# Performance work log

Measured on AMD Instinct MI355X. Metric: run time of the kernel, lower is better.

Reference implementation:

```python
import jax, jax.numpy as jnp
import numpy as np

B = 32768      # batch
D = 2          # input_dim
H = 2048       # hidden_dim
NQ = 4         # qubits


def setup_inputs() -> dict:
    key = jax.random.key(0)
    ks = jax.random.split(key, 14)

    def lin(k, fan_in, fan_out):
        # kaiming-uniform-ish init like nn.Linear
        bound = 1.0 / np.sqrt(fan_in)
        kw, kb = jax.random.split(k)
        W = jax.random.uniform(kw, (fan_in, fan_out), jnp.float32, -bound, bound)
        b = jax.random.uniform(kb, (fan_out,), jnp.float32, -bound, bound)
        return W, b

    x = jax.random.normal(ks[0], (B, D), jnp.float32)
    W1, b1 = lin(ks[1], D + NQ, H)      # core Linear 1
    W2, b2 = lin(ks[2], H, H)           # core Linear 2
    Wc, bc = lin(ks[3], H, 1)           # classifier
    Wr1, br1 = lin(ks[4], D, 8)
    Wr2, br2 = lin(ks[5], 8, 4)
    Wr3, br3 = lin(ks[6], 4, 1)
    return dict(x=x, W1=W1, b1=b1, W2=W2, b2=b2, Wc=Wc, bc=bc,
                Wr1=Wr1, br1=br1, Wr2=Wr2, br2=br2, Wr3=Wr3, br3=br3)


def _quantum_feature_map(x):
    # Exact closed form of: RY(x_i) on 4 qubits from |0000>, CNOT(0,1), CNOT(2,3),
    # expval(PauliZ(i)). Padding with zeros -> cos(0)=1 on unused wires.
    xq = jnp.pad(x, ((0, 0), (0, NQ - x.shape[1])))  # [B,4]
    c = jnp.cos(xq)
    return jnp.stack([c[:, 0], c[:, 0] * c[:, 1], c[:, 2], c[:, 2] * c[:, 3]], axis=1)


def reference(x, W1, b1, W2, b2, Wc, bc, Wr1, br1, Wr2, br2, Wr3, br3):
    qfeat = _quantum_feature_map(x)               # [B,4]
    concat = jnp.concatenate([x, qfeat], axis=1)  # [B, D+4]
    h = jnp.tanh(concat @ W1 + b1)                # [B,H]
    h = jnp.tanh(h @ W2 + b2)                     # [B,H]
    logits = h @ Wc + bc                          # [B,1]
    r = jnp.tanh(x @ Wr1 + br1)
    r = jnp.tanh(r @ Wr2 + br2)
    risk = r @ Wr3 + br3                          # [B,1]
    return logits, risk
```

## Files before the change

### kernel.cpp

```cpp
#include <hip/hip_runtime.h>
#include <hip/hip_bf16.h>
#include <stdint.h>

#define B_ROWS 32768
#define HID    2048
#define K_DIM  2048

#define BM 256
#define BN 256
#define BKB 128
#define NKT (K_DIM / BKB)
#define NS  4
#define NU  (NS * NKT)
#define ASTEP ((size_t)8192 * K_DIM)

#define SCALE_W   5747.3639f
#define DEQUANT   1.3700225e-6f

#define L1_BLOCKS (B_ROWS / 32)
#define TR_BLOCKS ((HID/32)*(K_DIM/32))

typedef int  int4v __attribute__((ext_vector_type(4)));
typedef char char8 __attribute__((ext_vector_type(8)));

__device__ __forceinline__ float fast_tanh(float x) {
    float e = __expf(2.0f * x);
    return 1.0f - 2.0f * __builtin_amdgcn_rcpf(e + 1.0f);
}

__device__ __forceinline__ void gl_lds16(const void* g, void* l) {
    __builtin_amdgcn_global_load_lds(
        (const __attribute__((address_space(1))) void*)(uintptr_t)g,
        (__attribute__((address_space(3))) void*)(uint32_t)(uintptr_t)l,
        16, 0, 0);
}

__global__ __launch_bounds__(256) void prep_kernel(
    const float* __restrict__ x,   const float* __restrict__ W1, const float* __restrict__ b1,
    const float* __restrict__ W2,
    const float* __restrict__ Wr1, const float* __restrict__ br1,
    const float* __restrict__ Wr2, const float* __restrict__ br2,
    const float* __restrict__ Wr3, const float* __restrict__ br3,
    const float* __restrict__ bc,
    char* __restrict__ h1, char* __restrict__ W2t, float* __restrict__ out) {
    const int t = threadIdx.x;
    if (blockIdx.x >= L1_BLOCKS) {
        __shared__ float tile[32][33];
        const int tb = blockIdx.x - L1_BLOCKS;
        const int n0 = (tb & 63) * 32;
        const int k0 = (tb >> 6) * 32;
        const int tx = t & 31;
        const int ty = t >> 5;
#pragma unroll
        for (int i = 0; i < 4; ++i) {
            int k = k0 + ty + i * 8;
            tile[ty + i * 8][tx] = W2[(size_t)k * HID + n0 + tx];
        }
        __syncthreads();
#pragma unroll
        for (int i = 0; i < 4; ++i) {
            int n = n0 + ty + i * 8;
            W2t[(size_t)n * K_DIM + k0 + tx] =
                (char)__float2int_rn(tile[tx][ty + i * 8] * SCALE_W);
        }
        return;
    }
    const int n0 = t * 8;
    float w0[8], w1[8], w2[8], w3[8], wb[8];
#pragma unroll
    for (int j = 0; j < 8; ++j) {
        w0[j] = W1[0 * HID + n0 + j];
        w1[j] = W1[1 * HID + n0 + j];
        w2[j] = W1[2 * HID + n0 + j];
        w3[j] = W1[3 * HID + n0 + j];
        wb[j] = W1[4 * HID + n0 + j] + W1[5 * HID + n0 + j] + b1[n0 + j];
    }
    const int brow0 = blockIdx.x * 32;
    for (int r = 0; r < 32; ++r) {
        const int b = brow0 + r;
        const float x0 = x[2 * b], x1 = x[2 * b + 1];
        const float c0 = __cosf(x0);
        const float cc = c0 * __cosf(x1);
        char8 v;
#pragma unroll
        for (int j = 0; j < 8; ++j) {
            float z = wb[j] + x0 * w0[j] + x1 * w1[j] + c0 * w2[j] + cc * w3[j];
            v[j] = (char)__float2int_rn(fast_tanh(z) * 127.0f);
        }
        *(char8*)(h1 + (size_t)b * HID + n0) = v;
    }
    if (t < 32) {
        const int b = brow0 + t;
        const float x0 = x[2 * b], x1 = x[2 * b + 1];
        float r1[8];
#pragma unroll
        for (int j = 0; j < 8; ++j)
            r1[j] = fast_tanh(br1[j] + x0 * Wr1[j] + x1 * Wr1[8 + j]);
        float r2[4];
#pragma unroll
        for (int j = 0; j < 4; ++j) {
            float s = br2[j];
#pragma unroll
            for (int i = 0; i < 8; ++i) s += r1[i] * Wr2[i * 4 + j];
            r2[j] = fast_tanh(s);
        }
        float risk = br3[0];
#pragma unroll
        for (int i = 0; i < 4; ++i) risk += r2[i] * Wr3[i];
        out[B_ROWS + b] = risk;
        out[b]          = bc[0];
    }
}

__global__ __launch_bounds__(512, 2) void gemm_kernel(
    const char* __restrict__ A,
    const char* __restrict__ Bt,
    const float* __restrict__ b2, const float* __restrict__ Wc,
    float* __restrict__ out) {
    __shared__ __align__(16) char sA[2][BM * BKB];
    __shared__ __align__(16) char sB[2][BN * BKB];

    const int tid  = threadIdx.x;
    const int wave = tid >> 6;
    const int lane = tid & 63;
    const int p    = blockIdx.x;
    const int n0   = (p & 7) * BN;
    const size_t m0base = (size_t)(p >> 3) * BM;

    const int rsub  = lane >> 3;
    const int chunk = (lane & 7) ^ rsub;
    const char* aS[4]; const char* bS[4]; uint32_t off4[4];
#pragma unroll
    for (int i = 0; i < 4; ++i) {
        int seg = (i >> 1) * 16 + wave * 2 + (i & 1);
        aS[i] = A  + (m0base + seg * 8 + rsub) * (size_t)K_DIM + chunk * 16;
        bS[i] = Bt + ((size_t)n0 + seg * 8 + rsub) * K_DIM + chunk * 16;
        off4[i] = seg * 1024;
    }

    const int wr   = wave >> 2;
    const int wc   = wave & 3;
    const int quad = lane >> 4;
    const int r16  = lane & 15;
    const int x7   = lane & 7;
    const int aRow = wr * 128 + r16;
    const int bRow = wc * 64  + r16;

    float b2v[4], wcv[4];
#pragma unroll
    for (int ni = 0; ni < 4; ++ni) {
        int gn = n0 + wc * 64 + ni * 16 + r16;
        b2v[ni] = b2[gn];
        wcv[ni] = Wc[gn];
    }

    int4v acc[8][4] = {};

    auto stage = [&](int u, char* dA, char* dB) {
        const size_t ao = (size_t)(u >> 4) * ASTEP + (size_t)(u & 15) * BKB;
        const size_t bo = (size_t)(u & 15) * BKB;
#pragma unroll
        for (int i = 0; i < 4; ++i) {
            gl_lds16(aS[i] + ao, dA + off4[i]);
            gl_lds16(bS[i] + bo, dB + off4[i]);
        }
    };

    auto compute = [&](const char* pA, const char* pB) {
#pragma unroll
        for (int ks = 0; ks < 2; ++ks) {
            const int slot = ((ks * 4 + quad) ^ x7) * 16;
            int4v bf[4], af[4];
#pragma unroll
            for (int ni = 0; ni < 4; ++ni)
                bf[ni] = *(const int4v*)(pB + (bRow + ni * 16) * BKB + slot);
#pragma unroll
            for (int mi = 0; mi < 4; ++mi)
                af[mi] = *(const int4v*)(pA + (aRow + mi * 16) * BKB + slot);
            __builtin_amdgcn_s_setprio(1);
#pragma unroll
            for (int mi = 0; mi < 4; ++mi)
#pragma unroll
                for (int ni = 0; ni < 4; ++ni)
                    acc[mi][ni] = __builtin_amdgcn_mfma_i32_16x16x64_i8(
                        af[mi], bf[ni], acc[mi][ni], 0, 0, 0);
            __builtin_amdgcn_s_setprio(0);
#pragma unroll
            for (int mi = 0; mi < 4; ++mi)
                af[mi] = *(const int4v*)(pA + (aRow + (4 + mi) * 16) * BKB + slot);
            __builtin_amdgcn_s_setprio(1);
#pragma unroll
            for (int mi = 0; mi < 4; ++mi)
#pragma unroll
                for (int ni = 0; ni < 4; ++ni)
                    acc[4 + mi][ni] = __builtin_amdgcn_mfma_i32_16x16x64_i8(
                        af[mi], bf[ni], acc[4 + mi][ni], 0, 0, 0);
            __builtin_amdgcn_s_setprio(0);
        }
    };

    auto epilogue = [&](int s) {
        const int gm0 = (int)m0base + s * 8192 + wr * 128;
#pragma unroll
        for (int mi = 0; mi < 8; ++mi) {
#pragma unroll
            for (int r = 0; r < 4; ++r) {
                int gm = gm0 + mi * 16 + quad * 4 + r;
                float rs = 0.f;
#pragma unroll
                for (int ni = 0; ni < 4; ++ni)
                    rs += fast_tanh((float)acc[mi][ni][r] * DEQUANT + b2v[ni]) * wcv[ni];
                rs += __shfl_xor(rs, 1);
                rs += __shfl_xor(rs, 2);
                rs += __shfl_xor(rs, 4);
                rs += __shfl_xor(rs, 8);
                if (r16 == 0) atomicAdd(&out[gm], rs);
            }
        }
    };

    stage(0, sA[0], sB[0]);
    __syncthreads();

#pragma unroll 2
    for (int u = 0; u < NU; ++u) {
        const int c = u & 1;
        if (u + 1 < NU) stage(u + 1, sA[c ^ 1], sB[c ^ 1]);
        __builtin_amdgcn_sched_barrier(0);
        compute(sA[c], sB[c]);
        __syncthreads();
        if ((u & 15) == 15) {
            epilogue(u >> 4);
#pragma unroll
            for (int mi = 0; mi < 8; ++mi)
#pragma unroll
                for (int ni = 0; ni < 4; ++ni)
                    acc[mi][ni] = int4v{0, 0, 0, 0};
        }
    }
}

extern "C" void kernel_launch(void* const* d_in, const int* in_sizes, int n_in,
                              void* d_out, int out_size, void* d_ws, size_t ws_size,
                              hipStream_t stream) {
    const float* x   = (const float*)d_in[0];
    const float* W1  = (const float*)d_in[1];
    const float* b1  = (const float*)d_in[2];
    const float* W2  = (const float*)d_in[3];
    const float* b2  = (const float*)d_in[4];
    const float* Wc  = (const float*)d_in[5];
    const float* bc  = (const float*)d_in[6];
    const float* Wr1 = (const float*)d_in[7];
    const float* br1 = (const float*)d_in[8];
    const float* Wr2 = (const float*)d_in[9];
    const float* br2 = (const float*)d_in[10];
    const float* Wr3 = (const float*)d_in[11];
    const float* br3 = (const float*)d_in[12];
    float* out = (float*)d_out;

    char* W2t = (char*)d_ws;
    char* h1  = (char*)d_ws + (size_t)4 * 1024 * 1024;

    prep_kernel<<<L1_BLOCKS + TR_BLOCKS, 256, 0, stream>>>(
        x, W1, b1, W2, Wr1, br1, Wr2, br2, Wr3, br3, bc, h1, W2t, out);
    gemm_kernel<<<256, 512, 0, stream>>>(h1, W2t, b2, Wc, out);
}
```

Before: 243.5 us.

## Split int8 GEMM main loop into four interleaved load/MFMA phases with explicit waitcnts

Restructures each K-step of the int8 GEMM into four quadrant phases. Each phase issues a slice of the next tile's global-to-LDS prefetch, reads only the LDS fragments it needs, then runs an MFMA cluster. Fine-grained s_waitcnt vmcnt/lgkmcnt and s_barrier replace the single __syncthreads per step, so memory traffic and LDS reads overlap with matrix math. It also moves the b2/Wc loads into the epilogue to cut register pressure. The cost is many more barriers per iteration, and hand-counted vmcnt values that must match the issued loads exactly or the kernel reads stale data.

```diff
diff --git a/kernel.cpp b/kernel.cpp
--- a/kernel.cpp
+++ b/kernel.cpp
@@ -34,6 +34,11 @@
         (__attribute__((address_space(3))) void*)(uint32_t)(uintptr_t)l,
         16, 0, 0);
 }
+
+#define ASM_VMCNT(n) asm volatile("s_waitcnt vmcnt(" #n ")" ::: "memory")
+#define ASM_LGKM0()  asm volatile("s_waitcnt lgkmcnt(0)" ::: "memory")
+#define SCHED_FENCE() __builtin_amdgcn_sched_barrier(0)
+#define BAR()        __builtin_amdgcn_s_barrier()
 
 __global__ __launch_bounds__(256) void prep_kernel(
     const float* __restrict__ x,   const float* __restrict__ W1, const float* __restrict__ b1,
@@ -117,8 +122,8 @@
     const char* __restrict__ Bt,
     const float* __restrict__ b2, const float* __restrict__ Wc,
     float* __restrict__ out) {
-    __shared__ __align__(16) char sA[2][BM * BKB];
-    __shared__ __align__(16) char sB[2][BN * BKB];
+    __shared__ __align__(16) char sAb[2][BM * BKB];
+    __shared__ __align__(16) char sBb[2][BN * BKB];
 
     const int tid  = threadIdx.x;
     const int wave = tid >> 6;
@@ -129,77 +134,46 @@
 
     const int rsub  = lane >> 3;
     const int chunk = (lane & 7) ^ rsub;
-    const char* aS[4]; const char* bS[4]; uint32_t off4[4];
-#pragma unroll
-    for (int i = 0; i < 4; ++i) {
-        int seg = (i >> 1) * 16 + wave * 2 + (i & 1);
-        aS[i] = A  + (m0base + seg * 8 + rsub) * (size_t)K_DIM + chunk * 16;
-        bS[i] = Bt + ((size_t)n0 + seg * 8 + rsub) * K_DIM + chunk * 16;
-        off4[i] = seg * 1024;
-    }
+
+    const int segA0 = (wave < 4) ? 2 * wave : 8 + 2 * wave;
+    const int segA1 = segA0 + 8;
+    const int segB0 = ((wave >> 1) << 3) + ((wave & 1) << 1);
+    const int segB1 = segB0 + 4;
+    const char* srcA0 = A  + (m0base + segA0 * 8 + rsub) * (size_t)K_DIM + chunk * 16;
+    const char* srcA1 = A  + (m0base + segA1 * 8 + rsub) * (size_t)K_DIM + chunk * 16;
+    const char* srcB0 = Bt + ((size_t)n0 + segB0 * 8 + rsub) * K_DIM + chunk * 16;
+    const char* srcB1 = Bt + ((size_t)n0 + segB1 * 8 + rsub) * K_DIM + chunk * 16;
 
     const int wr   = wave >> 2;
     const int wc   = wave & 3;
     const int quad = lane >> 4;
     const int r16  = lane & 15;
     const int x7   = lane & 7;
-    const int aRow = wr * 128 + r16;
-    const int bRow = wc * 64  + r16;
-
-    float b2v[4], wcv[4];
-#pragma unroll
-    for (int ni = 0; ni < 4; ++ni) {
-        int gn = n0 + wc * 64 + ni * 16 + r16;
-        b2v[ni] = b2[gn];
-        wcv[ni] = Wc[gn];
-    }
+    const uint32_t aRowB = (wr * 128 + r16) * BKB;
+    const uint32_t bRowB = (wc * 64  + r16) * BKB;
+    const int slot0 = ((0 * 4 + quad) ^ x7) * 16;
+    const int slot1 = ((1 * 4 + quad) ^ x7) * 16;
 
     int4v acc[8][4] = {};
-
-    auto stage = [&](int u, char* dA, char* dB) {
-        const size_t ao = (size_t)(u >> 4) * ASTEP + (size_t)(u & 15) * BKB;
-        const size_t bo = (size_t)(u & 15) * BKB;
-#pragma unroll
-        for (int i = 0; i < 4; ++i) {
-            gl_lds16(aS[i] + ao, dA + off4[i]);
-            gl_lds16(bS[i] + bo, dB + off4[i]);
-        }
+    int4v a[2][4], b0[2][2], b1[2][2];
+
+    auto aoff = [&](int u) {
+        return (size_t)(u >> 4) * ASTEP + (size_t)(u & 15) * BKB;
     };
-
-    auto compute = [&](const char* pA, const char* pB) {
-#pragma unroll
-        for (int ks = 0; ks < 2; ++ks) {
-            const int slot = ((ks * 4 + quad) ^ x7) * 16;
-            int4v bf[4], af[4];
-#pragma unroll
-            for (int ni = 0; ni < 4; ++ni)
-                bf[ni] = *(const int4v*)(pB + (bRow + ni * 16) * BKB + slot);
-#pragma unroll
-            for (int mi = 0; mi < 4; ++mi)
-                af[mi] = *(const int4v*)(pA + (aRow + mi * 16) * BKB + slot);
-            __builtin_amdgcn_s_setprio(1);
-#pragma unroll
-            for (int mi = 0; mi < 4; ++mi)
-#pragma unroll
-                for (int ni = 0; ni < 4; ++ni)
-                    acc[mi][ni] = __builtin_amdgcn_mfma_i32_16x16x64_i8(
-                        af[mi], bf[ni], acc[mi][ni], 0, 0, 0);
-            __builtin_amdgcn_s_setprio(0);
-#pragma unroll
-            for (int mi = 0; mi < 4; ++mi)
-                af[mi] = *(const int4v*)(pA + (aRow + (4 + mi) * 16) * BKB + slot);
-            __builtin_amdgcn_s_setprio(1);
-#pragma unroll
-            for (int mi = 0; mi < 4; ++mi)
-#pragma unroll
-                for (int ni = 0; ni < 4; ++ni)
-                    acc[4 + mi][ni] = __builtin_amdgcn_mfma_i32_16x16x64_i8(
-                        af[mi], bf[ni], acc[4 + mi][ni], 0, 0, 0);
-            __builtin_amdgcn_s_setprio(0);
-        }
+    auto boff = [&](int u) { return (size_t)(u & 15) * BKB; };
+    auto stg2 = [&](const char* src, char* dbuf, int seg, size_t ko) {
+        gl_lds16(src + ko, dbuf + seg * 1024);
+        gl_lds16(src + (size_t)8 * K_DIM + ko, dbuf + (seg + 1) * 1024);
     };
 
     auto epilogue = [&](int s) {
+        float b2v[4], wcv[4];
+#pragma unroll
+        for (int ni = 0; ni < 4; ++ni) {
+            int gn = n0 + wc * 64 + ni * 16 + r16;
+            b2v[ni] = b2[gn];
+            wcv[ni] = Wc[gn];
+        }
         const int gm0 = (int)m0base + s * 8192 + wr * 128;
 #pragma unroll
         for (int mi = 0; mi < 8; ++mi) {
@@ -219,18 +193,109 @@
         }
     };
 
-    stage(0, sA[0], sB[0]);
+    stg2(srcA0, sAb[0], segA0, aoff(0));
+    stg2(srcB0, sBb[0], segB0, boff(0));
+    stg2(srcB1, sBb[0], segB1, boff(0));
+    stg2(srcA1, sAb[0], segA1, aoff(0));
+    ASM_VMCNT(0);
     __syncthreads();
 
-#pragma unroll 2
     for (int u = 0; u < NU; ++u) {
-        const int c = u & 1;
-        if (u + 1 < NU) stage(u + 1, sA[c ^ 1], sB[c ^ 1]);
-        __builtin_amdgcn_sched_barrier(0);
-        compute(sA[c], sB[c]);
-        __syncthreads();
+        const int cur = u & 1;
+        const char* pA = sAb[cur];
+        const char* pB = sBb[cur];
+        char* dA = sAb[cur ^ 1];
+        char* dB = sBb[cur ^ 1];
+        const bool pf = (u + 1 < NU);
+        const size_t ao = pf ? aoff(u + 1) : 0;
+        const size_t bo = pf ? boff(u + 1) : 0;
+
+        ASM_VMCNT(4);
+#pragma unroll
+        for (int ks = 0; ks < 2; ++ks) {
+            const int slot = ks ? slot1 : slot0;
+#pragma unroll
+            for (int mi = 0; mi < 4; ++mi)
+                a[ks][mi] = *(const int4v*)(pA + aRowB + mi * 16 * BKB + slot);
+#pragma unroll
+            for (int ni = 0; ni < 2; ++ni)
+                b0[ks][ni] = *(const int4v*)(pB + bRowB + ni * 16 * BKB + slot);
+        }
+        if (pf) stg2(srcA0, dA, segA0, ao);
+        SCHED_FENCE(); BAR(); ASM_LGKM0(); SCHED_FENCE();
+        __builtin_amdgcn_s_setprio(1);
+#pragma unroll
+        for (int ks = 0; ks < 2; ++ks)
+#pragma unroll
+            for (int mi = 0; mi < 4; ++mi)
+#pragma unroll
+                for (int ni = 0; ni < 2; ++ni)
+                    acc[mi][ni] = __builtin_amdgcn_mfma_i32_16x16x64_i8(
+                        a[ks][mi], b0[ks][ni], acc[mi][ni], 0, 0, 0);
+        __builtin_amdgcn_s_setprio(0);
+        SCHED_FENCE(); BAR();
+
+        if (pf) { ASM_VMCNT(4); } else { ASM_VMCNT(2); }
+#pragma unroll
+        for (int ks = 0; ks < 2; ++ks) {
+            const int slot = ks ? slot1 : slot0;
+#pragma unroll
+            for (int ni = 0; ni < 2; ++ni)
+                b1[ks][ni] = *(const int4v*)(pB + bRowB + (2 + ni) * 16 * BKB + slot);
+        }
+        if (pf) stg2(srcB0, dB, segB0, bo);
+        SCHED_FENCE(); BAR(); ASM_LGKM0(); SCHED_FENCE();
+        __builtin_amdgcn_s_setprio(1);
+#pragma unroll
+        for (int ks = 0; ks < 2; ++ks)
+#pragma unroll
+            for (int mi = 0; mi < 4; ++mi)
+#pragma unroll
+                for (int ni = 0; ni < 2; ++ni)
+                    acc[mi][2 + ni] = __builtin_amdgcn_mfma_i32_16x16x64_i8(
+                        a[ks][mi], b1[ks][ni], acc[mi][2 + ni], 0, 0, 0);
+        __builtin_amdgcn_s_setprio(0);
+        SCHED_FENCE(); BAR();
+
+        if (pf) { ASM_VMCNT(4); } else { ASM_VMCNT(0); }
+#pragma unroll
+        for (int ks = 0; ks < 2; ++ks) {
+            const int slot = ks ? slot1 : slot0;
+#pragma unroll
+            for (int mi = 0; mi < 4; ++mi)
+                a[ks][mi] = *(const int4v*)(pA + aRowB + (4 + mi) * 16 * BKB + slot);
+        }
+        if (pf) stg2(srcB1, dB, segB1, bo);
+        SCHED_FENCE(); BAR(); ASM_LGKM0(); SCHED_FENCE();
+        __builtin_amdgcn_s_setprio(1);
+#pragma unroll
+        for (int ks = 0; ks < 2; ++ks)
+#pragma unroll
+            for (int mi = 0; mi < 4; ++mi)
+#pragma unroll
+                for (int ni = 0; ni < 2; ++ni)
+                    acc[4 + mi][ni] = __builtin_amdgcn_mfma_i32_16x16x64_i8(
+                        a[ks][mi], b0[ks][ni], acc[4 + mi][ni], 0, 0, 0);
+        __builtin_amdgcn_s_setprio(0);
+        SCHED_FENCE(); BAR();
+
+        if (pf) stg2(srcA1, dA, segA1, ao);
+        SCHED_FENCE(); BAR();
+        __builtin_amdgcn_s_setprio(1);
+#pragma unroll
+        for (int ks = 0; ks < 2; ++ks)
+#pragma unroll
+            for (int mi = 0; mi < 4; ++mi)
+#pragma unroll
+                for (int ni = 0; ni < 2; ++ni)
+                    acc[4 + mi][2 + ni] = __builtin_amdgcn_mfma_i32_16x16x64_i8(
+                        a[ks][mi], b1[ks][ni], acc[4 + mi][2 + ni], 0, 0, 0);
+        __builtin_amdgcn_s_setprio(0);
+        SCHED_FENCE(); BAR();
+
         if ((u & 15) == 15) {
             epilogue(u >> 4);
+            ASM_VMCNT(0);
 #pragma unroll
             for (int mi = 0; mi < 8; ++mi)
 #pragma unroll
```

Result: slower. 258.1 us (+6.0%).

## Load B weight fragments directly from global into registers, stage only A in LDS

Applied to the files above, without the earlier changes.

The GEMM kernel stops staging the B (W2 transposed) tile through shared memory. Each wave now loads its B fragments straight from global memory into registers, prefetching the next k-step, and only A is double-buffered in LDS. The wave layout changes from 2x4 to 4x2 so each wave covers 64 rows by 128 columns, with manual vmcnt waits and raw barriers replacing __syncthreads. This halves LDS traffic and footprint and could raise occupancy. In exchange it adds redundant global/L2 reads of B across blocks, more register pressure, and relies on hand-counted vmcnt ordering that could be fragile.

```diff
diff --git a/kernel.cpp b/kernel.cpp
--- a/kernel.cpp
+++ b/kernel.cpp
@@ -13,6 +13,7 @@
 #define NS  4
 #define NU  (NS * NKT)
 #define ASTEP ((size_t)8192 * K_DIM)
+#define NSTRIDE (16 * K_DIM)
 
 #define SCALE_W   5747.3639f
 #define DEQUANT   1.3700225e-6f
@@ -34,6 +35,10 @@
         (__attribute__((address_space(3))) void*)(uint32_t)(uintptr_t)l,
         16, 0, 0);
 }
+
+#define ASM_VMCNT(n) asm volatile("s_waitcnt vmcnt(" #n ")" ::: "memory")
+#define SCHED_FENCE() __builtin_amdgcn_sched_barrier(0)
+#define BAR()        __builtin_amdgcn_s_barrier()
 
 __global__ __launch_bounds__(256) void prep_kernel(
     const float* __restrict__ x,   const float* __restrict__ W1, const float* __restrict__ b1,
@@ -117,8 +122,7 @@
     const char* __restrict__ Bt,
     const float* __restrict__ b2, const float* __restrict__ Wc,
     float* __restrict__ out) {
-    __shared__ __align__(16) char sA[2][BM * BKB];
-    __shared__ __align__(16) char sB[2][BN * BKB];
+    __shared__ __align__(16) char sAb[2][BM * BKB];
 
     const int tid  = threadIdx.x;
     const int wave = tid >> 6;
@@ -129,86 +133,52 @@
 
     const int rsub  = lane >> 3;
     const int chunk = (lane & 7) ^ rsub;
-    const char* aS[4]; const char* bS[4]; uint32_t off4[4];
-#pragma unroll
-    for (int i = 0; i < 4; ++i) {
-        int seg = (i >> 1) * 16 + wave * 2 + (i & 1);
-        aS[i] = A  + (m0base + seg * 8 + rsub) * (size_t)K_DIM + chunk * 16;
-        bS[i] = Bt + ((size_t)n0 + seg * 8 + rsub) * K_DIM + chunk * 16;
-        off4[i] = seg * 1024;
-    }
-
-    const int wr   = wave >> 2;
-    const int wc   = wave & 3;
+    const char* srcA01 = A + (m0base + (size_t)(wave * 4 + 0) * 8 + rsub) * K_DIM + chunk * 16;
+    const char* srcA23 = A + (m0base + (size_t)(wave * 4 + 2) * 8 + rsub) * K_DIM + chunk * 16;
+    const uint32_t offA = (wave * 4) * 1024;
+
+    const int wr   = wave >> 1;
+    const int wc   = wave & 1;
     const int quad = lane >> 4;
     const int r16  = lane & 15;
     const int x7   = lane & 7;
-    const int aRow = wr * 128 + r16;
-    const int bRow = wc * 64  + r16;
-
-    float b2v[4], wcv[4];
-#pragma unroll
-    for (int ni = 0; ni < 4; ++ni) {
-        int gn = n0 + wc * 64 + ni * 16 + r16;
-        b2v[ni] = b2[gn];
-        wcv[ni] = Wc[gn];
-    }
-
-    int4v acc[8][4] = {};
-
-    auto stage = [&](int u, char* dA, char* dB) {
-        const size_t ao = (size_t)(u >> 4) * ASTEP + (size_t)(u & 15) * BKB;
-        const size_t bo = (size_t)(u & 15) * BKB;
-#pragma unroll
-        for (int i = 0; i < 4; ++i) {
-            gl_lds16(aS[i] + ao, dA + off4[i]);
-            gl_lds16(bS[i] + bo, dB + off4[i]);
-        }
+    const uint32_t aRowB = (wr * 64 + r16) * BKB;
+    const int slot0 = ((0 * 4 + quad) ^ x7) * 16;
+    const int slot1 = ((1 * 4 + quad) ^ x7) * 16;
+
+    const char* bBase = Bt + ((size_t)n0 + wc * 128 + r16) * K_DIM + quad * 16;
+
+    int4v acc[4][8] = {};
+    int4v a[4], b0[8], b1[8];
+
+    auto aoff = [&](int u) {
+        return (size_t)(u >> 4) * ASTEP + (size_t)(u & 15) * BKB;
     };
-
-    auto compute = [&](const char* pA, const char* pB) {
-#pragma unroll
-        for (int ks = 0; ks < 2; ++ks) {
-            const int slot = ((ks * 4 + quad) ^ x7) * 16;
-            int4v bf[4], af[4];
-#pragma unroll
-            for (int ni = 0; ni < 4; ++ni)
-                bf[ni] = *(const int4v*)(pB + (bRow + ni * 16) * BKB + slot);
-#pragma unroll
-            for (int mi = 0; mi < 4; ++mi)
-                af[mi] = *(const int4v*)(pA + (aRow + mi * 16) * BKB + slot);
-            __builtin_amdgcn_s_setprio(1);
-#pragma unroll
-            for (int mi = 0; mi < 4; ++mi)
-#pragma unroll
-                for (int ni = 0; ni < 4; ++ni)
-                    acc[mi][ni] = __builtin_amdgcn_mfma_i32_16x16x64_i8(
-                        af[mi], bf[ni], acc[mi][ni], 0, 0, 0);
-            __builtin_amdgcn_s_setprio(0);
-#pragma unroll
-            for (int mi = 0; mi < 4; ++mi)
-                af[mi] = *(const int4v*)(pA + (aRow + (4 + mi) * 16) * BKB + slot);
-            __builtin_amdgcn_s_setprio(1);
-#pragma unroll
-            for (int mi = 0; mi < 4; ++mi)
-#pragma unroll
-                for (int ni = 0; ni < 4; ++ni)
-                    acc[4 + mi][ni] = __builtin_amdgcn_mfma_i32_16x16x64_i8(
-                        af[mi], bf[ni], acc[4 + mi][ni], 0, 0, 0);
-            __builtin_amdgcn_s_setprio(0);
-        }
+    auto stageA = [&](int u, char* dA) {
+        const size_t ao = aoff(u);
+        gl_lds16(srcA01 + ao,                     dA + offA);
+        gl_lds16(srcA01 + (size_t)8 * K_DIM + ao, dA + offA + 1024);
+        gl_lds16(srcA23 + ao,                     dA + offA + 2048);
+        gl_lds16(srcA23 + (size_t)8 * K_DIM + ao, dA + offA + 3072);
     };
 
     auto epilogue = [&](int s) {
-        const int gm0 = (int)m0base + s * 8192 + wr * 128;
-#pragma unroll
-        for (int mi = 0; mi < 8; ++mi) {
+        float b2v[8], wcv[8];
+#pragma unroll
+        for (int ni = 0; ni < 8; ++ni) {
+            int gn = n0 + wc * 128 + ni * 16 + r16;
+            b2v[ni] = b2[gn];
+            wcv[ni] = Wc[gn];
+        }
+        const int gm0 = (int)m0base + s * 8192 + wr * 64;
+#pragma unroll
+        for (int mi = 0; mi < 4; ++mi) {
 #pragma unroll
             for (int r = 0; r < 4; ++r) {
                 int gm = gm0 + mi * 16 + quad * 4 + r;
                 float rs = 0.f;
 #pragma unroll
-                for (int ni = 0; ni < 4; ++ni)
+                for (int ni = 0; ni < 8; ++ni)
                     rs += fast_tanh((float)acc[mi][ni][r] * DEQUANT + b2v[ni]) * wcv[ni];
                 rs += __shfl_xor(rs, 1);
                 rs += __shfl_xor(rs, 2);
@@ -219,22 +189,67 @@
         }
     };
 
-    stage(0, sA[0], sB[0]);
+    stageA(0, sAb[0]);
+    ASM_VMCNT(0);
     __syncthreads();
-
-#pragma unroll 2
+#pragma unroll
+    for (int ni = 0; ni < 8; ++ni)
+        b0[ni] = *(const int4v*)(bBase + (size_t)ni * NSTRIDE);
+    SCHED_FENCE();
+
     for (int u = 0; u < NU; ++u) {
-        const int c = u & 1;
-        if (u + 1 < NU) stage(u + 1, sA[c ^ 1], sB[c ^ 1]);
-        __builtin_amdgcn_sched_barrier(0);
-        compute(sA[c], sB[c]);
-        __syncthreads();
+        const int cur = u & 1;
+        const char* pA = sAb[cur];
+        char* dA = sAb[cur ^ 1];
+        const int un  = (u + 1) & (NU - 1);
+        const size_t kb  = (size_t)(u  & 15) * BKB;
+        const size_t kbn = (size_t)(un & 15) * BKB;
+
+#pragma unroll
+        for (int ni = 0; ni < 8; ++ni)
+            b1[ni] = *(const int4v*)(bBase + (size_t)ni * NSTRIDE + kb + 64);
+        stageA(un, dA);
+#pragma unroll
+        for (int mi = 0; mi < 4; ++mi)
+            a[mi] = *(const int4v*)(pA + aRowB + mi * 16 * BKB + slot0);
+        SCHED_FENCE();
+
+        __builtin_amdgcn_s_setprio(1);
+#pragma unroll
+        for (int mi = 0; mi < 4; ++mi)
+#pragma unroll
+            for (int ni = 0; ni < 8; ++ni)
+                acc[mi][ni] = __builtin_amdgcn_mfma_i32_16x16x64_i8(
+                    a[mi], b0[ni], acc[mi][ni], 0, 0, 0);
+        __builtin_amdgcn_s_setprio(0);
+
+#pragma unroll
+        for (int mi = 0; mi < 4; ++mi)
+            a[mi] = *(const int4v*)(pA + aRowB + mi * 16 * BKB + slot1);
+#pragma unroll
+        for (int ni = 0; ni < 8; ++ni)
+            b0[ni] = *(const int4v*)(bBase + (size_t)ni * NSTRIDE + kbn);
+        SCHED_FENCE();
+
+        __builtin_amdgcn_s_setprio(1);
+#pragma unroll
+        for (int mi = 0; mi < 4; ++mi)
+#pragma unroll
+            for (int ni = 0; ni < 8; ++ni)
+                acc[mi][ni] = __builtin_amdgcn_mfma_i32_16x16x64_i8(
+                    a[mi], b1[ni], acc[mi][ni], 0, 0, 0);
+        __builtin_amdgcn_s_setprio(0);
+
+        ASM_VMCNT(8);
+        BAR();
+
         if ((u & 15) == 15) {
             epilogue(u >> 4);
-#pragma unroll
-            for (int mi = 0; mi < 8; ++mi)
-#pragma unroll
-                for (int ni = 0; ni < 4; ++ni)
+            ASM_VMCNT(0);
+#pragma unroll
+            for (int mi = 0; mi < 4; ++mi)
+#pragma unroll
+                for (int ni = 0; ni < 8; ++ni)
                     acc[mi][ni] = int4v{0, 0, 0, 0};
         }
     }
```

Result: slower. 387.4 us (+59.1%).
